# Performance work log

Hardware: AMD Instinct MI355X
Metric: run time of the kernel (lower is better)

## Reference

```python
import jax, jax.numpy as jnp
import numpy as np

NOT_EPSILON = 1.0

def swishmax(x, axis):
    # x * exp(x - max) normalized by sum(|.|) + 1 over `axis`
    xexp = x * jnp.exp(x - jnp.max(x, axis=axis, keepdims=True))
    return xexp / (jnp.sum(jnp.abs(xexp), axis=axis, keepdims=True) + NOT_EPSILON)

def setup_inputs() -> dict:
    key = jax.random.key(0)
    ks = jax.random.split(key, 8)
    B, S, D = 2, 512, 256
    std = 0.02
    x = jax.random.normal(ks[0], (B, S, D), dtype=jnp.float32)
    w_pre = jax.random.normal(ks[1], (D, D), dtype=jnp.float32) * std
    w_q   = jax.random.normal(ks[2], (D, D), dtype=jnp.float32) * std
    w_k   = jax.random.normal(ks[3], (D, D), dtype=jnp.float32) * std
    w_va  = jax.random.normal(ks[4], (D, D), dtype=jnp.float32) * std
    w_al  = jax.random.normal(ks[5], (D, D), dtype=jnp.float32) * std
    w_vo  = jax.random.normal(ks[6], (D, D), dtype=jnp.float32) * std
    w_end = jax.random.normal(ks[7], (D, D), dtype=jnp.float32) * std
    return {"x": x, "w_pre": w_pre, "w_q": w_q, "w_k": w_k,
            "w_va": w_va, "w_al": w_al, "w_vo": w_vo, "w_end": w_end}

def reference(x, w_pre, w_q, w_k, w_va, w_al, w_vo, w_end):
    # pre: module_1d = Linear(D, D, bias=False)
    X = x @ w_pre.T                                    # [B,S,D]
    # FractalAttention depth=2 (base case): row_dims=(-3,)
    q = X + X @ w_q.T                                  # residual query proj
    k = X + X @ w_k.T                                  # residual key proj
    # batchify: key lhs -> [B,Sk,1,D], query rhs -> [B,1,Sq,D]
    raw = k[:, :, None, :] * q[:, None, :, :]          # [B,Sk,Sq,D]
    logits = raw + raw @ w_al.T                        # residual logit proj over D
    scale = swishmax(logits, axis=-3)                  # normalize over Sk
    v = X + X @ w_va.T
    vs = v[:, :, None, :] * scale                      # [B,Sk,Sq,D]
    vsum = jnp.sum(vs, axis=-3)                        # [B,Sq,D]
    vout = vsum + vsum @ w_vo.T
    X = X + vout                                       # transformer residual
    X = X @ w_end.T                                    # end: module_1d
    return X
```

## Files before the change

### kernel.cpp

```cpp
#include <hip/hip_runtime.h>
#include <hip/hip_bf16.h>


typedef __attribute__((ext_vector_type(8))) short short8;
typedef __attribute__((ext_vector_type(4))) float f32x4;

#define DD 256
#define SS 512
#define KVB 32
#define LOG2E 1.4426950408889634f
#define LN2   0.6931471805599453f

__device__ __forceinline__ unsigned short f2bf(float f) {
  unsigned int b = __float_as_uint(f);
  b += 0x7FFFu + ((b >> 16) & 1u);
  return (unsigned short)(b >> 16);
}
__device__ __forceinline__ float bf2f(unsigned short u) {
  return __uint_as_float(((unsigned int)u) << 16);
}
__device__ __forceinline__ short8 cvt8(f32x4 lo, f32x4 hi) {
  short8 r;
  r[0]=(short)f2bf(lo[0]); r[1]=(short)f2bf(lo[1]);
  r[2]=(short)f2bf(lo[2]); r[3]=(short)f2bf(lo[3]);
  r[4]=(short)f2bf(hi[0]); r[5]=(short)f2bf(hi[1]);
  r[6]=(short)f2bf(hi[2]); r[7]=(short)f2bf(hi[3]);
  return r;
}
__device__ __forceinline__ void gload16(const void* g, void* l) {
  __builtin_amdgcn_global_load_lds(
      (const __attribute__((address_space(1))) void*)g,
      (__attribute__((address_space(3))) void*)l,
      16, 0, 0);
}

__global__ __launch_bounds__(256) void prep_weights(
    const float* __restrict__ w0, const float* __restrict__ w1,
    const float* __restrict__ w2, const float* __restrict__ w3,
    const float* __restrict__ w4, const float* __restrict__ w5,
    const float* __restrict__ wal, unsigned short* __restrict__ out)
{
  const int bi = blockIdx.x;
  const int m = bi >> 5;
  const int off = ((bi & 31) * 256 + threadIdx.x) * 8;
  const float* src = m==0?w0: m==1?w1: m==2?w2: m==3?w3: m==4?w4: m==5?w5: wal;
  f32x4 a = *(const f32x4*)(src + off);
  f32x4 b = *(const f32x4*)(src + off + 4);
  if (m == 6) {
    const int e = off >> 8, d = off & 255;
#pragma unroll
    for (int jj = 0; jj < 4; ++jj) {
      if (e == d + jj)     a[jj] += 1.0f;
      if (e == d + 4 + jj) b[jj] += 1.0f;
    }
  }
  *(short8*)(out + (size_t)m * 65536 + off) = cvt8(a, b);
}

__global__ __launch_bounds__(256) void linear_bf(
    const float* __restrict__ A, const unsigned short* __restrict__ Wbf,
    const float* __restrict__ res1, const float* __restrict__ res2,
    float* __restrict__ out)
{
  const int bi = blockIdx.x;
  const int rb = (bi >> 2) * 16;
  const int cb = (bi & 3) * 64;
  const int tid = threadIdx.x;
  const int wv = tid >> 6, lane = tid & 63;
  const int g = lane >> 4, c = lane & 15;
  const int arow = rb + c;
  const int wrow = cb + wv * 16 + c;

  f32x4 acc = (f32x4){0.f, 0.f, 0.f, 0.f};
#pragma unroll
  for (int ks = 0; ks < 8; ++ks) {
    const int d0 = ks * 32 + g * 8;
    f32x4 a0 = *(const f32x4*)(A + arow * DD + d0);
    f32x4 a1 = *(const f32x4*)(A + arow * DD + d0 + 4);
    short8 av = cvt8(a0, a1);
    short8 bv = *(const short8*)(Wbf + wrow * DD + d0);
    acc = __builtin_amdgcn_mfma_f32_16x16x32_bf16(av, bv, acc, 0, 0, 0);
  }
#pragma unroll
  for (int j = 0; j < 4; ++j) {
    const int ro = rb + g * 4 + j;
    const int co = cb + wv * 16 + c;
    float v = acc[j];
    if (res1) v += res1[ro * DD + co];
    if (res2) v += res2[ro * DD + co];
    out[ro * DD + co] = v;
  }
}

__global__ __launch_bounds__(256) void linear_qkv(
    const float* __restrict__ X,
    const unsigned short* __restrict__ Wq, const unsigned short* __restrict__ Wk,
    const unsigned short* __restrict__ Wv,
    float* __restrict__ qout, unsigned short* __restrict__ kout,
    float* __restrict__ vout)
{
  const int bi = blockIdx.x;
  const int rb = (bi >> 2) * 16;
  const int cb = (bi & 3) * 64;
  const int tid = threadIdx.x;
  const int wv = tid >> 6, lane = tid & 63;
  const int g = lane >> 4, c = lane & 15;
  const int arow = rb + c;
  const int wrow = cb + wv * 16 + c;

  f32x4 aq = (f32x4){0.f,0.f,0.f,0.f};
  f32x4 ak = (f32x4){0.f,0.f,0.f,0.f};
  f32x4 av_ = (f32x4){0.f,0.f,0.f,0.f};
#pragma unroll
  for (int ks = 0; ks < 8; ++ks) {
    const int d0 = ks * 32 + g * 8;
    f32x4 a0 = *(const f32x4*)(X + arow * DD + d0);
    f32x4 a1 = *(const f32x4*)(X + arow * DD + d0 + 4);
    short8 af = cvt8(a0, a1);
    short8 bq = *(const short8*)(Wq + wrow * DD + d0);
    aq = __builtin_amdgcn_mfma_f32_16x16x32_bf16(af, bq, aq, 0, 0, 0);
    short8 bk = *(const short8*)(Wk + wrow * DD + d0);
    ak = __builtin_amdgcn_mfma_f32_16x16x32_bf16(af, bk, ak, 0, 0, 0);
    short8 bv = *(const short8*)(Wv + wrow * DD + d0);
    av_ = __builtin_amdgcn_mfma_f32_16x16x32_bf16(af, bv, av_, 0, 0, 0);
  }
#pragma unroll
  for (int j = 0; j < 4; ++j) {
    const int ro = rb + g * 4 + j;
    const int co = cb + wv * 16 + c;
    const float base = X[ro * DD + co];
    qout[ro * DD + co] = (base + aq[j]) * LOG2E;
    kout[ro * DD + co] = f2bf(base + ak[j]);
    vout[ro * DD + co] = base + av_[j];
  }
}

__global__ __launch_bounds__(256, 3) void fractal_attn(
    const unsigned short* __restrict__ walI,
    const float* __restrict__ q,
    const unsigned short* __restrict__ kbf,
    const float* __restrict__ vf,
    float* __restrict__ vsum)
{
  __shared__ char smem[2][16384];

  const int wg = blockIdx.x;
  const int eh = wg & 1;
  const int sq = (wg >> 1) & 511;
  const int b  = wg >> 10;
  const int tid = threadIdx.x;
  const int wv = tid >> 6, lane = tid & 63;
  const int g = lane >> 4, c = lane & 15;

  const unsigned short* kbase = kbf + (size_t)b * SS * DD;
  int srco[4];
#pragma unroll
  for (int it = 0; it < 4; ++it) {
    const int p = it * 256 + tid;
    const int row = p >> 5, gc = p & 31;
    srco[it] = row * DD + (gc ^ (row & 7)) * 8;
  }
  auto stage = [&](int t) {
    char* dst = (char*)smem[t & 1];
    const unsigned short* ks = kbase + t * KVB * DD;
#pragma unroll
    for (int it = 0; it < 4; ++it)
      gload16(ks + srco[it], dst + (it * 256 + tid) * 16);
  };

  stage(0);

  short8 afrag[2][8];
  {
    const float* qrow = q + (size_t)(b * SS + sq) * DD;
#pragma unroll
    for (int i = 0; i < 2; ++i) {
      const int e = eh * 128 + wv * 32 + i * 16 + c;
      const unsigned short* wrow = walI + (size_t)e * DD;
#pragma unroll
      for (int ks = 0; ks < 8; ++ks) {
        const int d0 = ks * 32 + g * 8;
        short8 w8 = *(const short8*)(wrow + d0);
        f32x4 q0 = *(const f32x4*)(qrow + d0);
        f32x4 q1 = *(const f32x4*)(qrow + d0 + 4);
        f32x4 lo, hi;
        lo[0] = bf2f((unsigned short)w8[0]) * q0[0];
        lo[1] = bf2f((unsigned short)w8[1]) * q0[1];
        lo[2] = bf2f((unsigned short)w8[2]) * q0[2];
        lo[3] = bf2f((unsigned short)w8[3]) * q0[3];
        hi[0] = bf2f((unsigned short)w8[4]) * q1[0];
        hi[1] = bf2f((unsigned short)w8[5]) * q1[1];
        hi[2] = bf2f((unsigned short)w8[6]) * q1[2];
        hi[3] = bf2f((unsigned short)w8[7]) * q1[3];
        afrag[i][ks] = cvt8(lo, hi);
      }
    }
  }

  const int kbA = c * 512 + ((g ^ (c & 3)) << 4) + (((c >> 2) & 1) << 6);
  const int kbB = kbA ^ 64;

  const float* vwg = vf + (size_t)b * SS * DD;
  int voffe[2][2];
#pragma unroll
  for (int n = 0; n < 2; ++n)
#pragma unroll
    for (int i = 0; i < 2; ++i)
      voffe[n][i] = (n * 16 + c) * DD + eh * 128 + wv * 32 + i * 16 + g * 4;

  float mst[8], sst[8], vst[8];
#pragma unroll
  for (int s = 0; s < 8; ++s) { mst[s] = -1e30f; sst[s] = 0.f; vst[s] = 0.f; }

  for (int t = 0; t < 16; ++t) {
    __syncthreads();

    const float* vt = vwg + (size_t)t * KVB * DD;
    f32x4 vv[2][2];
#pragma unroll
    for (int n = 0; n < 2; ++n)
#pragma unroll
      for (int i = 0; i < 2; ++i)
        vv[n][i] = *(const f32x4*)(vt + voffe[n][i]);
    if (t < 15) stage(t + 1);

    const char* kb = (const char*)smem[t & 1];
    f32x4 acc[2][2];
#pragma unroll
    for (int i = 0; i < 2; ++i)
#pragma unroll
      for (int n = 0; n < 2; ++n) acc[i][n] = (f32x4){0.f,0.f,0.f,0.f};

#pragma unroll
    for (int ks2 = 0; ks2 < 4; ++ks2) {
      short8 bA0 = *(const short8*)(kb + kbA + ks2 * 128);
      short8 bA1 = *(const short8*)(kb + kbA + ks2 * 128 + 8192);
      acc[0][0] = __builtin_amdgcn_mfma_f32_16x16x32_bf16(afrag[0][2*ks2], bA0, acc[0][0], 0, 0, 0);
      acc[1][0] = __builtin_amdgcn_mfma_f32_16x16x32_bf16(afrag[1][2*ks2], bA0, acc[1][0], 0, 0, 0);
      acc[0][1] = __builtin_amdgcn_mfma_f32_16x16x32_bf16(afrag[0][2*ks2], bA1, acc[0][1], 0, 0, 0);
      acc[1][1] = __builtin_amdgcn_mfma_f32_16x16x32_bf16(afrag[1][2*ks2], bA1, acc[1][1], 0, 0, 0);
      short8 bB0 = *(const short8*)(kb + kbB + ks2 * 128);
      short8 bB1 = *(const short8*)(kb + kbB + ks2 * 128 + 8192);
      acc[0][0] = __builtin_amdgcn_mfma_f32_16x16x32_bf16(afrag[0][2*ks2+1], bB0, acc[0][0], 0, 0, 0);
      acc[1][0] = __builtin_amdgcn_mfma_f32_16x16x32_bf16(afrag[1][2*ks2+1], bB0, acc[1][0], 0, 0, 0);
      acc[0][1] = __builtin_amdgcn_mfma_f32_16x16x32_bf16(afrag[0][2*ks2+1], bB1, acc[0][1], 0, 0, 0);
      acc[1][1] = __builtin_amdgcn_mfma_f32_16x16x32_bf16(afrag[1][2*ks2+1], bB1, acc[1][1], 0, 0, 0);
    }

#pragma unroll
    for (int i = 0; i < 2; ++i) {
#pragma unroll
      for (int j = 0; j < 4; ++j) {
        const int s = i * 4 + j;
        const float L0 = acc[i][0][j], L1 = acc[i][1][j];
        mst[s] = fmaxf(fmaxf(mst[s], L0), L1);
        const float e0 = __builtin_amdgcn_exp2f(L0);
        const float e1 = __builtin_amdgcn_exp2f(L1);
        const float p0 = L0 * e0, p1 = L1 * e1;
        sst[s] += fabsf(p0) + fabsf(p1);
        vst[s] = fmaf(vv[0][i][j], p0, vst[s]);
        vst[s] = fmaf(vv[1][i][j], p1, vst[s]);
      }
    }
  }

#pragma unroll
  for (int mask = 1; mask <= 8; mask <<= 1) {
#pragma unroll
    for (int s = 0; s < 8; ++s) {
      mst[s] = fmaxf(mst[s], __shfl_xor(mst[s], mask));
      sst[s] += __shfl_xor(sst[s], mask);
      vst[s] += __shfl_xor(vst[s], mask);
    }
  }

  if (c == 0) {
    float* orow = vsum + (size_t)(b * SS + sq) * DD;
#pragma unroll
    for (int i = 0; i < 2; ++i) {
      f32x4 o;
#pragma unroll
      for (int j = 0; j < 4; ++j) {
        const int s = i * 4 + j;
        const float tt = LN2 * __builtin_amdgcn_exp2f(-mst[s]);
        o[j] = vst[s] * tt / (sst[s] * tt + 1.0f);
      }
      *(f32x4*)(orow + eh * 128 + wv * 32 + i * 16 + g * 4) = o;
    }
  }
}

extern "C" void kernel_launch(void* const* d_in, const int* in_sizes, int n_in,
                              void* d_out, int out_size, void* d_ws, size_t ws_size,
                              hipStream_t stream) {
  const float* x     = (const float*)d_in[0];
  const float* w_pre = (const float*)d_in[1];
  const float* w_q   = (const float*)d_in[2];
  const float* w_k   = (const float*)d_in[3];
  const float* w_va  = (const float*)d_in[4];
  const float* w_al  = (const float*)d_in[5];
  const float* w_vo  = (const float*)d_in[6];
  const float* w_end = (const float*)d_in[7];
  float* out = (float*)d_out;

  char* ws = (char*)d_ws;
  float* X    = (float*)(ws);
  float* q    = (float*)(ws + (1 << 20));
  float* vsum = (float*)(ws + (2 << 20));
  float* Y    = (float*)(ws + (3 << 20));
  unsigned short* k_bf = (unsigned short*)(ws + (4 << 20));
  float* v_f32         = (float*)(ws + (4 << 20) + (512 << 10));
  unsigned short* wbf  = (unsigned short*)(ws + (5 << 20) + (512 << 10));

  prep_weights<<<224, 256, 0, stream>>>(w_pre, w_q, w_k, w_va, w_vo, w_end,
                                        w_al, wbf);
  linear_bf<<<256, 256, 0, stream>>>(x, wbf + 0 * 65536, nullptr, nullptr, X);
  linear_qkv<<<256, 256, 0, stream>>>(X, wbf + 1 * 65536, wbf + 2 * 65536,
                                      wbf + 3 * 65536, q, k_bf, v_f32);
  fractal_attn<<<2048, 256, 0, stream>>>(wbf + 6 * 65536, q, k_bf, v_f32, vsum);
  linear_bf<<<256, 256, 0, stream>>>(vsum, wbf + 4 * 65536, vsum, X, Y);
  linear_bf<<<256, 256, 0, stream>>>(Y, wbf + 5 * 65536, nullptr, nullptr, out);
}
```

Measured before the change: 127.5 us.

## Process full feature dim per workgroup and store v in bf16

Each attention workgroup now covers all 256 output features for one query row instead of half, so K tiles staged in shared memory are reused across twice as many MFMAs and K traffic is halved. The grid halves to 1024 blocks. The v projection is stored as bf16 to halve v load bandwidth, and the launch-bounds occupancy hint rises to 8. The cost is doubled register state per thread (afrag, accumulators, running stats), which the higher occupancy target may force into spills. There is also a small precision loss in v.

```diff
diff --git a/kernel.cpp b/kernel.cpp
--- a/kernel.cpp
+++ b/kernel.cpp
@@ -4,6 +4,7 @@
 
 typedef __attribute__((ext_vector_type(8))) short short8;
 typedef __attribute__((ext_vector_type(4))) float f32x4;
+typedef __attribute__((ext_vector_type(4))) unsigned short ushort4v;
 
 #define DD 256
 #define SS 512
@@ -97,7 +98,7 @@
     const unsigned short* __restrict__ Wq, const unsigned short* __restrict__ Wk,
     const unsigned short* __restrict__ Wv,
     float* __restrict__ qout, unsigned short* __restrict__ kout,
-    float* __restrict__ vout)
+    unsigned short* __restrict__ vout)
 {
   const int bi = blockIdx.x;
   const int rb = (bi >> 2) * 16;
@@ -131,23 +132,22 @@
     const float base = X[ro * DD + co];
     qout[ro * DD + co] = (base + aq[j]) * LOG2E;
     kout[ro * DD + co] = f2bf(base + ak[j]);
-    vout[ro * DD + co] = base + av_[j];
-  }
-}
-
-__global__ __launch_bounds__(256, 3) void fractal_attn(
+    vout[ro * DD + co] = f2bf(base + av_[j]);
+  }
+}
+
+__global__ __launch_bounds__(256, 8) void fractal_attn(
     const unsigned short* __restrict__ walI,
     const float* __restrict__ q,
     const unsigned short* __restrict__ kbf,
-    const float* __restrict__ vf,
+    const unsigned short* __restrict__ vbf,
     float* __restrict__ vsum)
 {
   __shared__ char smem[2][16384];
 
   const int wg = blockIdx.x;
-  const int eh = wg & 1;
-  const int sq = (wg >> 1) & 511;
-  const int b  = wg >> 10;
+  const int sq = wg & 511;
+  const int b  = wg >> 9;
   const int tid = threadIdx.x;
   const int wv = tid >> 6, lane = tid & 63;
   const int g = lane >> 4, c = lane & 15;
@@ -170,12 +170,12 @@
 
   stage(0);
 
-  short8 afrag[2][8];
+  short8 afrag[4][8];
   {
     const float* qrow = q + (size_t)(b * SS + sq) * DD;
 #pragma unroll
-    for (int i = 0; i < 2; ++i) {
-      const int e = eh * 128 + wv * 32 + i * 16 + c;
+    for (int i = 0; i < 4; ++i) {
+      const int e = wv * 64 + i * 16 + c;
       const unsigned short* wrow = walI + (size_t)e * DD;
 #pragma unroll
       for (int ks = 0; ks < 8; ++ks) {
@@ -200,66 +200,77 @@
   const int kbA = c * 512 + ((g ^ (c & 3)) << 4) + (((c >> 2) & 1) << 6);
   const int kbB = kbA ^ 64;
 
-  const float* vwg = vf + (size_t)b * SS * DD;
-  int voffe[2][2];
-#pragma unroll
-  for (int n = 0; n < 2; ++n)
-#pragma unroll
-    for (int i = 0; i < 2; ++i)
-      voffe[n][i] = (n * 16 + c) * DD + eh * 128 + wv * 32 + i * 16 + g * 4;
-
-  float mst[8], sst[8], vst[8];
-#pragma unroll
-  for (int s = 0; s < 8; ++s) { mst[s] = -1e30f; sst[s] = 0.f; vst[s] = 0.f; }
+  const unsigned short* vbase = vbf + (size_t)b * SS * DD;
+  const int vofbase = c * DD + wv * 64 + g * 4;
+
+  float mst[16], sst[16], vst[16];
+#pragma unroll
+  for (int s = 0; s < 16; ++s) { mst[s] = -1e30f; sst[s] = 0.f; vst[s] = 0.f; }
+
+  const f32x4 zeroc = (f32x4){0.f, 0.f, 0.f, 0.f};
 
   for (int t = 0; t < 16; ++t) {
     __syncthreads();
 
-    const float* vt = vwg + (size_t)t * KVB * DD;
-    f32x4 vv[2][2];
+    const unsigned short* vt = vbase + (size_t)t * KVB * DD;
+    ushort4v vq[2][4];
 #pragma unroll
     for (int n = 0; n < 2; ++n)
 #pragma unroll
-      for (int i = 0; i < 2; ++i)
-        vv[n][i] = *(const f32x4*)(vt + voffe[n][i]);
+      for (int i = 0; i < 4; ++i)
+        vq[n][i] = *(const ushort4v*)(vt + vofbase + n * 16 * DD + i * 16);
     if (t < 15) stage(t + 1);
 
     const char* kb = (const char*)smem[t & 1];
-    f32x4 acc[2][2];
-#pragma unroll
-    for (int i = 0; i < 2; ++i)
-#pragma unroll
-      for (int n = 0; n < 2; ++n) acc[i][n] = (f32x4){0.f,0.f,0.f,0.f};
-
-#pragma unroll
-    for (int ks2 = 0; ks2 < 4; ++ks2) {
+    f32x4 acc[4][2];
+
+    {
+      short8 bA0 = *(const short8*)(kb + kbA);
+      short8 bA1 = *(const short8*)(kb + kbA + 8192);
+#pragma unroll
+      for (int i = 0; i < 4; ++i) {
+        acc[i][0] = __builtin_amdgcn_mfma_f32_16x16x32_bf16(afrag[i][0], bA0, zeroc, 0, 0, 0);
+        acc[i][1] = __builtin_amdgcn_mfma_f32_16x16x32_bf16(afrag[i][0], bA1, zeroc, 0, 0, 0);
+      }
+      short8 bB0 = *(const short8*)(kb + kbB);
+      short8 bB1 = *(const short8*)(kb + kbB + 8192);
+#pragma unroll
+      for (int i = 0; i < 4; ++i) {
+        acc[i][0] = __builtin_amdgcn_mfma_f32_16x16x32_bf16(afrag[i][1], bB0, acc[i][0], 0, 0, 0);
+        acc[i][1] = __builtin_amdgcn_mfma_f32_16x16x32_bf16(afrag[i][1], bB1, acc[i][1], 0, 0, 0);
+      }
+    }
+#pragma unroll
+    for (int ks2 = 1; ks2 < 4; ++ks2) {
       short8 bA0 = *(const short8*)(kb + kbA + ks2 * 128);
       short8 bA1 = *(const short8*)(kb + kbA + ks2 * 128 + 8192);
-      acc[0][0] = __builtin_amdgcn_mfma_f32_16x16x32_bf16(afrag[0][2*ks2], bA0, acc[0][0], 0, 0, 0);
-      acc[1][0] = __builtin_amdgcn_mfma_f32_16x16x32_bf16(afrag[1][2*ks2], bA0, acc[1][0], 0, 0, 0);
-      acc[0][1] = __builtin_amdgcn_mfma_f32_16x16x32_bf16(afrag[0][2*ks2], bA1, acc[0][1], 0, 0, 0);
-      acc[1][1] = __builtin_amdgcn_mfma_f32_16x16x32_bf16(afrag[1][2*ks2], bA1, acc[1][1], 0, 0, 0);
+#pragma unroll
+      for (int i = 0; i < 4; ++i) {
+        acc[i][0] = __builtin_amdgcn_mfma_f32_16x16x32_bf16(afrag[i][2*ks2], bA0, acc[i][0], 0, 0, 0);
+        acc[i][1] = __builtin_amdgcn_mfma_f32_16x16x32_bf16(afrag[i][2*ks2], bA1, acc[i][1], 0, 0, 0);
+      }
       short8 bB0 = *(const short8*)(kb + kbB + ks2 * 128);
       short8 bB1 = *(const short8*)(kb + kbB + ks2 * 128 + 8192);
-      acc[0][0] = __builtin_amdgcn_mfma_f32_16x16x32_bf16(afrag[0][2*ks2+1], bB0, acc[0][0], 0, 0, 0);
-      acc[1][0] = __builtin_amdgcn_mfma_f32_16x16x32_bf16(afrag[1][2*ks2+1], bB0, acc[1][0], 0, 0, 0);
-      acc[0][1] = __builtin_amdgcn_mfma_f32_16x16x32_bf16(afrag[0][2*ks2+1], bB1, acc[0][1], 0, 0, 0);
-      acc[1][1] = __builtin_amdgcn_mfma_f32_16x16x32_bf16(afrag[1][2*ks2+1], bB1, acc[1][1], 0, 0, 0);
-    }
-
-#pragma unroll
-    for (int i = 0; i < 2; ++i) {
-#pragma unroll
-      for (int j = 0; j < 4; ++j) {
-        const int s = i * 4 + j;
-        const float L0 = acc[i][0][j], L1 = acc[i][1][j];
-        mst[s] = fmaxf(fmaxf(mst[s], L0), L1);
-        const float e0 = __builtin_amdgcn_exp2f(L0);
-        const float e1 = __builtin_amdgcn_exp2f(L1);
-        const float p0 = L0 * e0, p1 = L1 * e1;
-        sst[s] += fabsf(p0) + fabsf(p1);
-        vst[s] = fmaf(vv[0][i][j], p0, vst[s]);
-        vst[s] = fmaf(vv[1][i][j], p1, vst[s]);
+#pragma unroll
+      for (int i = 0; i < 4; ++i) {
+        acc[i][0] = __builtin_amdgcn_mfma_f32_16x16x32_bf16(afrag[i][2*ks2+1], bB0, acc[i][0], 0, 0, 0);
+        acc[i][1] = __builtin_amdgcn_mfma_f32_16x16x32_bf16(afrag[i][2*ks2+1], bB1, acc[i][1], 0, 0, 0);
+      }
+    }
+
+#pragma unroll
+    for (int n = 0; n < 2; ++n) {
+#pragma unroll
+      for (int i = 0; i < 4; ++i) {
+#pragma unroll
+        for (int j = 0; j < 4; ++j) {
+          const int s = i * 4 + j;
+          const float L = acc[i][n][j];
+          mst[s] = fmaxf(mst[s], L);
+          const float p = L * __builtin_amdgcn_exp2f(L);
+          sst[s] += fabsf(p);
+          vst[s] = fmaf(bf2f((unsigned short)vq[n][i][j]), p, vst[s]);
+        }
       }
     }
   }
@@ -267,7 +278,7 @@
 #pragma unroll
   for (int mask = 1; mask <= 8; mask <<= 1) {
 #pragma unroll
-    for (int s = 0; s < 8; ++s) {
+    for (int s = 0; s < 16; ++s) {
       mst[s] = fmaxf(mst[s], __shfl_xor(mst[s], mask));
       sst[s] += __shfl_xor(sst[s], mask);
       vst[s] += __shfl_xor(vst[s], mask);
@@ -277,7 +288,7 @@
   if (c == 0) {
     float* orow = vsum + (size_t)(b * SS + sq) * DD;
 #pragma unroll
-    for (int i = 0; i < 2; ++i) {
+    for (int i = 0; i < 4; ++i) {
       f32x4 o;
 #pragma unroll
       for (int j = 0; j < 4; ++j) {
@@ -285,7 +296,7 @@
         const float tt = LN2 * __builtin_amdgcn_exp2f(-mst[s]);
         o[j] = vst[s] * tt / (sst[s] * tt + 1.0f);
       }
-      *(f32x4*)(orow + eh * 128 + wv * 32 + i * 16 + g * 4) = o;
+      *(f32x4*)(orow + wv * 64 + i * 16 + g * 4) = o;
     }
   }
 }
@@ -309,15 +320,15 @@
   float* vsum = (float*)(ws + (2 << 20));
   float* Y    = (float*)(ws + (3 << 20));
   unsigned short* k_bf = (unsigned short*)(ws + (4 << 20));
-  float* v_f32         = (float*)(ws + (4 << 20) + (512 << 10));
-  unsigned short* wbf  = (unsigned short*)(ws + (5 << 20) + (512 << 10));
+  unsigned short* v_bf = (unsigned short*)(ws + (4 << 20) + (512 << 10));
+  unsigned short* wbf  = (unsigned short*)(ws + (5 << 20));
 
   prep_weights<<<224, 256, 0, stream>>>(w_pre, w_q, w_k, w_va, w_vo, w_end,
                                         w_al, wbf);
   linear_bf<<<256, 256, 0, stream>>>(x, wbf + 0 * 65536, nullptr, nullptr, X);
   linear_qkv<<<256, 256, 0, stream>>>(X, wbf + 1 * 65536, wbf + 2 * 65536,
-                                      wbf + 3 * 65536, q, k_bf, v_f32);
-  fractal_attn<<<2048, 256, 0, stream>>>(wbf + 6 * 65536, q, k_bf, v_f32, vsum);
+                                      wbf + 3 * 65536, q, k_bf, v_bf);
+  fractal_attn<<<1024, 256, 0, stream>>>(wbf + 6 * 65536, q, k_bf, v_bf, vsum);
   linear_bf<<<256, 256, 0, stream>>>(vsum, wbf + 4 * 65536, vsum, X, Y);
   linear_bf<<<256, 256, 0, stream>>>(Y, wbf + 5 * 65536, nullptr, nullptr, out);
 }
```

After: 206.9 us. 1.62x slower.
